# Performance work log

Hardware: AMD Instinct MI355X
Metric: run time of the kernel (lower is better)

## Reference

```python
import jax, jax.numpy as jnp
import numpy as np

B, S, I, H = 32, 1024, 128, 128
D = 2 * H  # bidirectional concat feature dim


def setup_inputs() -> dict:
    key = jax.random.key(0)
    ks = jax.random.split(key, 12)
    lim = 1.0 / np.sqrt(H)  # PyTorch LSTMCell uniform init bound
    u = lambda k, shape: jax.random.uniform(k, shape, jnp.float32, -lim, lim)
    x = jax.random.normal(ks[0], (B, S, I), jnp.float32)
    return {
        "x": x,
        "fw_Wih": u(ks[1], (4 * H, I)), "fw_Whh": u(ks[2], (4 * H, H)),
        "fw_bih": u(ks[3], (4 * H,)),   "fw_bhh": u(ks[4], (4 * H,)),
        "bw_Wih": u(ks[5], (4 * H, I)), "bw_Whh": u(ks[6], (4 * H, H)),
        "bw_bih": u(ks[7], (4 * H,)),   "bw_bhh": u(ks[8], (4 * H,)),
        "Wq": u(ks[9], (D, D)), "Wk": u(ks[10], (D, D)), "Wv": u(ks[11], (D, D)),
    }


def _lstm_dir(x, Wih, Whh, bih, bhh):
    # x: [B, S, I] -> hidden states [B, S, H]; PyTorch LSTMCell gate math.
    xg = jnp.einsum('bsi,gi->bsg', x, Wih) + bih + bhh  # precompute input projections

    def step(carry, xg_t):
        h, c = carry
        g = xg_t + h @ Whh.T
        i_, f_, g_, o_ = jnp.split(g, 4, axis=-1)
        c = jax.nn.sigmoid(f_) * c + jax.nn.sigmoid(i_) * jnp.tanh(g_)
        h = jax.nn.sigmoid(o_) * jnp.tanh(c)
        return (h, c), h

    h0 = jnp.zeros((x.shape[0], Whh.shape[1]), x.dtype)
    _, hs = jax.lax.scan(step, (h0, h0), jnp.swapaxes(xg, 0, 1))
    return jnp.swapaxes(hs, 0, 1)


def reference(x, fw_Wih, fw_Whh, fw_bih, fw_bhh,
              bw_Wih, bw_Whh, bw_bih, bw_bhh, Wq, Wk, Wv):
    f_h = _lstm_dir(x, fw_Wih, fw_Whh, fw_bih, fw_bhh)            # [B,S,H]
    b_h = _lstm_dir(x[:, ::-1, :], bw_Wih, bw_Whh, bw_bih, bw_bhh)[:, ::-1, :]
    h = jnp.concatenate([f_h, b_h], axis=2)                        # [B,S,2H]
    q = h @ Wq.T
    k = h @ Wk.T
    v = h @ Wv.T
    att = jnp.einsum('bsd,btd->bst', q, k) / jnp.sqrt(jnp.asarray(D, h.dtype))
    att = jax.nn.softmax(att, axis=2)
    return jnp.einsum('bst,btd->bsd', att, v)
```

## Files before the change

kernel.cpp:

```cpp
#include <hip/hip_runtime.h>

typedef unsigned short u16;
typedef unsigned int u32;
typedef __bf16 bf16x8 __attribute__((ext_vector_type(8)));
typedef bf16x8 __attribute__((may_alias)) bf16x8a;
typedef float f32x4 __attribute__((ext_vector_type(4)));
typedef _Float16 f16;
typedef _Float16 f16x2 __attribute__((ext_vector_type(2)));

#define BB 32
#define SS 1024
#define HH 128
#define DD 256

__device__ __forceinline__ float b2f(u16 u) {
    u32 v = ((u32)u) << 16;
    return __builtin_bit_cast(float, v);
}
__device__ __forceinline__ u16 f2b(float f) {
    u32 u = __builtin_bit_cast(u32, f);
    u32 r = (u + 0x7fffu + ((u >> 16) & 1u)) >> 16;
    return (u16)r;
}
__device__ __forceinline__ float sig_fast(float x) {
    return __builtin_amdgcn_rcpf(1.0f + __builtin_amdgcn_exp2f(-1.4426950408889634f * x));
}
__device__ __forceinline__ float tanh_fast(float x) {
    return 2.0f * sig_fast(2.0f * x) - 1.0f;
}
template <int CTRL>
__device__ __forceinline__ float dpp_xor(float x) {
    return __builtin_bit_cast(float,
        __builtin_amdgcn_update_dpp(0, __builtin_bit_cast(int, x),
                                    CTRL, 0xF, 0xF, true));
}
__device__ __forceinline__ void lds_barrier() {
    asm volatile("s_waitcnt lgkmcnt(0)\n\ts_barrier" ::: "memory");
}

__global__ __launch_bounds__(256) void conv_weights(
    const float* __restrict__ fwWih, const float* __restrict__ bwWih,
    const float* __restrict__ fwWhh, const float* __restrict__ bwWhh,
    const float* __restrict__ Wq, const float* __restrict__ Wk,
    const float* __restrict__ Wv,
    u16* __restrict__ wfih, u16* __restrict__ wbih, u16* __restrict__ whhf,
    u16* __restrict__ wq, u16* __restrict__ wk, u16* __restrict__ wv)
{
    const int which = blockIdx.y;
    const float* src; u16* dst; int mode;
    switch (which) {
        case 0: src = fwWih; dst = wfih;              mode = 0; break;
        case 1: src = bwWih; dst = wbih;              mode = 0; break;
        case 2: src = fwWhh; dst = whhf;              mode = 1; break;
        case 3: src = bwWhh; dst = whhf + 512 * 128;  mode = 1; break;
        case 4: src = Wq;    dst = wq;                mode = 2; break;
        case 5: src = Wk;    dst = wk;                mode = 2; break;
        default: src = Wv;   dst = wv;                mode = 2; break;
    }
    for (int i = blockIdx.x * 256 + threadIdx.x; i < 65536 / 4; i += 32 * 256) {
        float4 v = ((const float4*)src)[i];
        ushort4 o;
        if (mode == 1) {
            o.x = __builtin_bit_cast(u16, (f16)v.x);
            o.y = __builtin_bit_cast(u16, (f16)v.y);
            o.z = __builtin_bit_cast(u16, (f16)v.z);
            o.w = __builtin_bit_cast(u16, (f16)v.w);
        } else {
            o.x = f2b(v.x); o.y = f2b(v.y); o.z = f2b(v.z); o.w = f2b(v.w);
        }
        if (mode == 2) {
            ((ushort4*)dst)[i] = o;
        } else {
            int r = i >> 5, c4 = i & 31;
            int rp = ((r & 127) << 2) | (r >> 7);
            *(ushort4*)&dst[rp * 128 + c4 * 4] = o;
        }
    }
}

template <int MODE, int AFP32>
__device__ __forceinline__ void gemm_core(
    const void* __restrict__ Araw, const u16* __restrict__ Bt,
    const float* __restrict__ bias1, const float* __restrict__ bias2,
    u16* __restrict__ Cout, int K, int N)
{
    __shared__ u16 As[128 * 72];
    __shared__ u16 Bs[128 * 72];
    const int tid = threadIdx.x;
    const int lane = tid & 63, wave = tid >> 6;
    const int wm = wave >> 1, wn = wave & 1;
    const int lo = lane & 15, hi = lane >> 4;
    const int m0 = blockIdx.x * 128, n0 = blockIdx.y * 128;

    f32x4 acc[4][4] = {};

    for (int k0 = 0; k0 < K; k0 += 64) {
        __syncthreads();
#pragma unroll
        for (int i = 0; i < 4; i++) {
            int c = tid + 256 * i;
            int row = c >> 3, kc = (c & 7) * 8;
            if (AFP32) {
                const float* ap = (const float*)Araw + (size_t)(m0 + row) * K + k0 + kc;
                float4 v0 = *(const float4*)ap;
                float4 v1 = *(const float4*)(ap + 4);
                uint4 o;
                o.x = (u32)f2b(v0.x) | ((u32)f2b(v0.y) << 16);
                o.y = (u32)f2b(v0.z) | ((u32)f2b(v0.w) << 16);
                o.z = (u32)f2b(v1.x) | ((u32)f2b(v1.y) << 16);
                o.w = (u32)f2b(v1.z) | ((u32)f2b(v1.w) << 16);
                *(uint4*)&As[row * 72 + kc] = o;
            } else {
                *(uint4*)&As[row * 72 + kc] =
                    *(const uint4*)&((const u16*)Araw)[(size_t)(m0 + row) * K + k0 + kc];
            }
            *(uint4*)&Bs[row * 72 + kc] =
                *(const uint4*)&Bt[(size_t)(n0 + row) * K + k0 + kc];
        }
        __syncthreads();
#pragma unroll
        for (int ks = 0; ks < 2; ks++) {
            bf16x8 af[4], bfr[4];
#pragma unroll
            for (int i = 0; i < 4; i++)
                af[i] = *(const bf16x8a*)&As[(wm * 64 + i * 16 + lo) * 72 + ks * 32 + hi * 8];
#pragma unroll
            for (int j = 0; j < 4; j++)
                bfr[j] = *(const bf16x8a*)&Bs[(wn * 64 + j * 16 + lo) * 72 + ks * 32 + hi * 8];
#pragma unroll
            for (int i = 0; i < 4; i++)
#pragma unroll
                for (int j = 0; j < 4; j++)
                    acc[i][j] = __builtin_amdgcn_mfma_f32_16x16x32_bf16(
                        af[i], bfr[j], acc[i][j], 0, 0, 0);
        }
    }
#pragma unroll
    for (int j = 0; j < 4; j++) {
        int col = n0 + wn * 64 + j * 16 + lo;
        float bsum = 0.f;
        if (MODE == 1) {
            int co = ((col & 3) << 7) | (col >> 2);
            bsum = bias1[co] + bias2[co];
        }
#pragma unroll
        for (int i = 0; i < 4; i++) {
            int row0 = m0 + wm * 64 + i * 16 + hi * 4;
#pragma unroll
            for (int r = 0; r < 4; r++) {
                float v = acc[i][j][r] + bsum;
                if (MODE == 1) {
                    int row = row0 + r;
                    int sidx = row & 1023, bidx = row >> 10;
                    Cout[(size_t)sidx * (BB * 512) + bidx * 512 + col] = f2b(v);
                } else {
                    Cout[(size_t)(row0 + r) * N + col] = f2b(v);
                }
            }
        }
    }
}

__global__ __launch_bounds__(256) void gemm_xg(
    const float* __restrict__ A, const u16* __restrict__ Bt_f,
    const u16* __restrict__ Bt_b,
    const float* __restrict__ f_bih, const float* __restrict__ f_bhh,
    const float* __restrict__ b_bih, const float* __restrict__ b_bhh,
    u16* __restrict__ xg)
{
    const int dir = blockIdx.z;
    gemm_core<1, 1>(A, dir ? Bt_b : Bt_f,
                    dir ? b_bih : f_bih, dir ? b_bhh : f_bhh,
                    xg + (size_t)dir * SS * BB * 512, 128, 512);
}

__global__ __launch_bounds__(256) void gemm_qkv(
    const u16* __restrict__ A, const u16* __restrict__ Wq,
    const u16* __restrict__ Wk, const u16* __restrict__ Wv,
    u16* __restrict__ qb, u16* __restrict__ kb, u16* __restrict__ vb)
{
    const int z = blockIdx.z;
    const u16* Bt = (z == 0) ? Wq : (z == 1) ? Wk : Wv;
    u16* out = (z == 0) ? qb : (z == 1) ? kb : vb;
    gemm_core<0, 0>(A, Bt, nullptr, nullptr, out, 256, 256);
}

__global__ __launch_bounds__(256)
__attribute__((amdgpu_waves_per_eu(1, 1)))
void lstm_scan_sk(
    const u16* __restrict__ Whh_h,
    const u16* __restrict__ xg,
    u16* __restrict__ hout)
{
    const int wg = blockIdx.x;
    const int dir = wg >> 5, b = wg & 31;
    const int t_ = threadIdx.x;
    const int u = t_ >> 1;
    const int kh = t_ & 1;

    u32 w[4][32];
    {
        const volatile u32* vp = (const volatile u32*)(Whh_h + (size_t)dir * 512 * 128);
#pragma unroll
        for (int g = 0; g < 4; g++) {
            int base = ((4 * u + g) * 128 + kh * 64) >> 1;
#pragma unroll
            for (int k = 0; k < 32; k++) w[g][k] = vp[base + k];
        }
    }

    __shared__ __align__(16) u16 hbuf[2][128];
    if (t_ < 128) hbuf[0][t_] = 0;
    float c = 0.0f;

    const u16* xgp = xg + (size_t)dir * SS * (BB * 512) + (size_t)b * 512 + 4 * u;
    u16* hop = hout + (size_t)b * SS * DD + dir * HH + u;

    int s = dir ? (SS - 1) : 0;
    const int d1 = dir ? -1 : 1;
    uint2 nxA = *(const uint2*)&xgp[(size_t)s * (BB * 512)];
    uint2 nxB = *(const uint2*)&xgp[(size_t)(s + d1) * (BB * 512)];
    lds_barrier();

    auto body = [&](uint2& nx, int parity) {
        uint2 xv = nx;
        int sp = s + 2 * d1;
        if ((unsigned)sp < SS)
            nx = *(const uint2*)&xgp[(size_t)sp * (BB * 512)];

        const uint4* hb = (const uint4*)&hbuf[parity][kh * 64];
        float g0 = 0.f, g1 = 0.f, g2 = 0.f, g3 = 0.f;
#pragma unroll
        for (int cc = 0; cc < 8; cc++) {
            uint4 hh = hb[cc];
            u32 hv[4] = {hh.x, hh.y, hh.z, hh.w};
#pragma unroll
            for (int j = 0; j < 4; j++) {
                f16x2 hp = __builtin_bit_cast(f16x2, hv[j]);
                g0 = __builtin_amdgcn_fdot2(hp, __builtin_bit_cast(f16x2, w[0][4 * cc + j]), g0, false);
                g1 = __builtin_amdgcn_fdot2(hp, __builtin_bit_cast(f16x2, w[1][4 * cc + j]), g1, false);
                g2 = __builtin_amdgcn_fdot2(hp, __builtin_bit_cast(f16x2, w[2][4 * cc + j]), g2, false);
                g3 = __builtin_amdgcn_fdot2(hp, __builtin_bit_cast(f16x2, w[3][4 * cc + j]), g3, false);
            }
        }
        g0 += dpp_xor<0xB1>(g0);
        g1 += dpp_xor<0xB1>(g1);
        g2 += dpp_xor<0xB1>(g2);
        g3 += dpp_xor<0xB1>(g3);
        g0 += b2f((u16)(xv.x & 0xffff)); g1 += b2f((u16)(xv.x >> 16));
        g2 += b2f((u16)(xv.y & 0xffff)); g3 += b2f((u16)(xv.y >> 16));

        c = fmaf(sig_fast(g1), c, sig_fast(g0) * tanh_fast(g2));
        float h = sig_fast(g3) * tanh_fast(c);

        if (kh == 0)
            hbuf[parity ^ 1][u] = __builtin_bit_cast(u16, (f16)h);
        else
            hop[(size_t)s * DD] = f2b(h);
        lds_barrier();
        s += d1;
    };

    for (int t = 0; t < SS; t += 2) {
        body(nxA, 0);
        body(nxB, 1);
    }
}

__global__ __launch_bounds__(256) void transpose_v(
    const u16* __restrict__ v, u16* __restrict__ vT)
{
    __shared__ u16 tile[64 * 72];
    const int b = blockIdx.z, s0 = blockIdx.x * 64, d0 = blockIdx.y * 64;
    const int tid = threadIdx.x;
#pragma unroll
    for (int i = 0; i < 2; i++) {
        int c = tid + 256 * i;
        int sl = c >> 3, dc = (c & 7) * 8;
        *(uint4*)&tile[sl * 72 + dc] =
            *(const uint4*)&v[((size_t)b * SS + s0 + sl) * DD + d0 + dc];
    }
    __syncthreads();
#pragma unroll
    for (int i = 0; i < 2; i++) {
        int c = tid + 256 * i;
        int dl = c >> 3, sc = (c & 7) * 8;
        u32 x0 = (u32)tile[(sc + 0) * 72 + dl] | ((u32)tile[(sc + 1) * 72 + dl] << 16);
        u32 x1 = (u32)tile[(sc + 2) * 72 + dl] | ((u32)tile[(sc + 3) * 72 + dl] << 16);
        u32 x2 = (u32)tile[(sc + 4) * 72 + dl] | ((u32)tile[(sc + 5) * 72 + dl] << 16);
        u32 x3 = (u32)tile[(sc + 6) * 72 + dl] | ((u32)tile[(sc + 7) * 72 + dl] << 16);
        uint4 val; val.x = x0; val.y = x1; val.z = x2; val.w = x3;
        *(uint4*)&vT[((size_t)b * DD + d0 + dl) * SS + s0 + sc] = val;
    }
}

__global__ __launch_bounds__(256) void attn_kernel(
    const u16* __restrict__ q, const u16* __restrict__ k,
    const u16* __restrict__ vT, float* __restrict__ out)
{
    __shared__ u16 Ks[32 * 264];
    __shared__ u16 Vs[256 * 40];
    __shared__ u16 Ps[64 * 40];
    const int bid = blockIdx.x;
    const int b = (bid & 7) * 4 + (bid >> 7);
    const int q0 = ((bid >> 3) & 15) * 64;
    const int tid = threadIdx.x, wave = tid >> 6, lane = tid & 63;
    const int lo = lane & 15, hi = lane >> 4;
    const float c1 = 0.09016844005556021f;

    bf16x8 qf[8];
    {
        const u16* qp = q + ((size_t)b * SS + q0 + wave * 16 + lo) * DD;
#pragma unroll
        for (int ks = 0; ks < 8; ks++)
            qf[ks] = *(const bf16x8a*)&qp[ks * 32 + hi * 8];
    }
    float m_i[4] = {-1e30f, -1e30f, -1e30f, -1e30f};
    float l_i[4] = {0.f, 0.f, 0.f, 0.f};
    f32x4 o[16] = {};

    for (int t0 = 0; t0 < SS; t0 += 32) {
        __syncthreads();
#pragma unroll
        for (int i = 0; i < 4; i++) {
            int c = tid + 256 * i;
            {
                int row = c >> 5, dc = (c & 31) * 8;
                *(uint4*)&Ks[row * 264 + dc] =
                    *(const uint4*)&k[((size_t)b * SS + t0 + row) * DD + dc];
            }
            {
                int d = c >> 2, sc = (c & 3) * 8;
                *(uint4*)&Vs[d * 40 + sc] =
                    *(const uint4*)&vT[((size_t)b * DD + d) * SS + t0 + sc];
            }
        }
        __syncthreads();

        f32x4 sacc[2] = {};
#pragma unroll
        for (int ks = 0; ks < 8; ks++) {
#pragma unroll
            for (int j = 0; j < 2; j++) {
                bf16x8 bfr = *(const bf16x8a*)&Ks[(j * 16 + lo) * 264 + ks * 32 + hi * 8];
                sacc[j] = __builtin_amdgcn_mfma_f32_16x16x32_bf16(qf[ks], bfr, sacc[j], 0, 0, 0);
            }
        }

        float tt[2][4];
#pragma unroll
        for (int j = 0; j < 2; j++)
#pragma unroll
            for (int r = 0; r < 4; r++) tt[j][r] = sacc[j][r] * c1;
        float rm[4];
#pragma unroll
        for (int r = 0; r < 4; r++) rm[r] = fmaxf(tt[0][r], tt[1][r]);
#pragma unroll
        for (int mm = 1; mm <= 8; mm <<= 1)
#pragma unroll
            for (int r = 0; r < 4; r++) rm[r] = fmaxf(rm[r], __shfl_xor(rm[r], mm, 64));
        float al[4], rs[4];
#pragma unroll
        for (int r = 0; r < 4; r++) {
            float mn = fmaxf(m_i[r], rm[r]);
            al[r] = __builtin_amdgcn_exp2f(m_i[r] - mn);
            m_i[r] = mn;
            rs[r] = 0.f;
        }
#pragma unroll
        for (int j = 0; j < 2; j++)
#pragma unroll
            for (int r = 0; r < 4; r++) {
                float p = __builtin_amdgcn_exp2f(tt[j][r] - m_i[r]);
                rs[r] += p;
                Ps[(wave * 16 + hi * 4 + r) * 40 + j * 16 + lo] = f2b(p);
            }
#pragma unroll
        for (int mm = 1; mm <= 8; mm <<= 1)
#pragma unroll
            for (int r = 0; r < 4; r++) rs[r] += __shfl_xor(rs[r], mm, 64);
#pragma unroll
        for (int r = 0; r < 4; r++) l_i[r] = l_i[r] * al[r] + rs[r];
#pragma unroll
        for (int nt = 0; nt < 16; nt++) {
            o[nt][0] *= al[0]; o[nt][1] *= al[1];
            o[nt][2] *= al[2]; o[nt][3] *= al[3];
        }
        __syncthreads();
        bf16x8 pa = *(const bf16x8a*)&Ps[(wave * 16 + lo) * 40 + hi * 8];
#pragma unroll
        for (int nt = 0; nt < 16; nt++) {
            bf16x8 bv = *(const bf16x8a*)&Vs[(nt * 16 + lo) * 40 + hi * 8];
            o[nt] = __builtin_amdgcn_mfma_f32_16x16x32_bf16(pa, bv, o[nt], 0, 0, 0);
        }
    }
    float inv[4];
#pragma unroll
    for (int r = 0; r < 4; r++) inv[r] = __builtin_amdgcn_rcpf(l_i[r]);
#pragma unroll
    for (int nt = 0; nt < 16; nt++)
#pragma unroll
        for (int r = 0; r < 4; r++) {
            int row = q0 + wave * 16 + hi * 4 + r;
            int col = nt * 16 + lo;
            out[((size_t)b * SS + row) * DD + col] = o[nt][r] * inv[r];
        }
}

extern "C" void kernel_launch(void* const* d_in, const int* in_sizes, int n_in,
                              void* d_out, int out_size, void* d_ws, size_t ws_size,
                              hipStream_t stream)
{
    (void)in_sizes; (void)n_in; (void)out_size;
    const float* x      = (const float*)d_in[0];
    const float* fw_Wih = (const float*)d_in[1];
    const float* fw_Whh = (const float*)d_in[2];
    const float* fw_bih = (const float*)d_in[3];
    const float* fw_bhh = (const float*)d_in[4];
    const float* bw_Wih = (const float*)d_in[5];
    const float* bw_Whh = (const float*)d_in[6];
    const float* bw_bih = (const float*)d_in[7];
    const float* bw_bhh = (const float*)d_in[8];
    const float* Wq = (const float*)d_in[9];
    const float* Wk = (const float*)d_in[10];
    const float* Wv = (const float*)d_in[11];

    if (ws_size < 143523840ULL) return;

    char* ws = (char*)d_ws;
    u16* xg  = (u16*)ws;
    u16* h   = (u16*)(ws + 67108864);
    u16* qb  = (u16*)(ws + 83886080);
    u16* kb  = (u16*)(ws + 100663296);
    u16* vT  = (u16*)(ws + 117440512);
    u16* wfih16 = (u16*)(ws + 142606336);
    u16* wbih16 = (u16*)(ws + 142606336 + 131072);
    u16* wq16   = (u16*)(ws + 142606336 + 262144);
    u16* wk16   = (u16*)(ws + 142606336 + 393216);
    u16* wv16   = (u16*)(ws + 142606336 + 524288);
    u16* whhf16 = (u16*)(ws + 142606336 + 655360);
    u16* vb = (u16*)ws;

    conv_weights<<<dim3(32, 7), 256, 0, stream>>>(
        fw_Wih, bw_Wih, fw_Whh, bw_Whh, Wq, Wk, Wv,
        wfih16, wbih16, whhf16, wq16, wk16, wv16);

    gemm_xg<<<dim3(256, 4, 2), 256, 0, stream>>>(
        x, wfih16, wbih16, fw_bih, fw_bhh, bw_bih, bw_bhh, xg);
    lstm_scan_sk<<<64, 256, 0, stream>>>(whhf16, xg, h);
    gemm_qkv<<<dim3(256, 2, 3), 256, 0, stream>>>(h, wq16, wk16, wv16, qb, kb, vb);
    transpose_v<<<dim3(16, 4, 32), 256, 0, stream>>>(vb, vT);
    attn_kernel<<<512, 256, 0, stream>>>(qb, kb, vT, (float*)d_out);
}
```

Before: 764.8 us.

## Compute V transposed directly in QKV GEMM and drop transpose kernel

The V projection is now computed as Wv·hᵀ by swapping the GEMM operands and transposing the grid mapping, so it writes V in [D, B*S] layout directly. This removes the separate transpose_v kernel and its extra read and write of V, and the attention kernel's V load indexing is updated to match. It also raises wave priority around the MFMA loops in the attention kernel with s_setprio. The risk is poorer coalescing in the new V layout load and the priority hints interacting badly with scheduling.

Result: faster. 744.6 us (-2.6%).

```diff
diff --git a/kernel.cpp b/kernel.cpp
--- a/kernel.cpp
+++ b/kernel.cpp
@@ -78,7 +78,7 @@
     }
 }
 
-template <int MODE, int AFP32>
+template <int MODE, int AFP32, int TRANSGRID = 0>
 __device__ __forceinline__ void gemm_core(
     const void* __restrict__ Araw, const u16* __restrict__ Bt,
     const float* __restrict__ bias1, const float* __restrict__ bias2,
@@ -90,7 +90,8 @@
     const int lane = tid & 63, wave = tid >> 6;
     const int wm = wave >> 1, wn = wave & 1;
     const int lo = lane & 15, hi = lane >> 4;
-    const int m0 = blockIdx.x * 128, n0 = blockIdx.y * 128;
+    const int m0 = (TRANSGRID ? blockIdx.y : blockIdx.x) * 128;
+    const int n0 = (TRANSGRID ? blockIdx.x : blockIdx.y) * 128;
 
     f32x4 acc[4][4] = {};
 
@@ -177,12 +178,16 @@
 __global__ __launch_bounds__(256) void gemm_qkv(
     const u16* __restrict__ A, const u16* __restrict__ Wq,
     const u16* __restrict__ Wk, const u16* __restrict__ Wv,
-    u16* __restrict__ qb, u16* __restrict__ kb, u16* __restrict__ vb)
+    u16* __restrict__ qb, u16* __restrict__ kb, u16* __restrict__ vT)
 {
     const int z = blockIdx.z;
-    const u16* Bt = (z == 0) ? Wq : (z == 1) ? Wk : Wv;
-    u16* out = (z == 0) ? qb : (z == 1) ? kb : vb;
-    gemm_core<0, 0>(A, Bt, nullptr, nullptr, out, 256, 256);
+    if (z == 2) {
+        gemm_core<0, 0, 1>(Wv, A, nullptr, nullptr, vT, 256, BB * SS);
+    } else {
+        const u16* Bt = (z == 0) ? Wq : Wk;
+        u16* out = (z == 0) ? qb : kb;
+        gemm_core<0, 0>(A, Bt, nullptr, nullptr, out, 256, 256);
+    }
 }
 
 __global__ __launch_bounds__(256)
@@ -264,33 +269,6 @@
     for (int t = 0; t < SS; t += 2) {
         body(nxA, 0);
         body(nxB, 1);
-    }
-}
-
-__global__ __launch_bounds__(256) void transpose_v(
-    const u16* __restrict__ v, u16* __restrict__ vT)
-{
-    __shared__ u16 tile[64 * 72];
-    const int b = blockIdx.z, s0 = blockIdx.x * 64, d0 = blockIdx.y * 64;
-    const int tid = threadIdx.x;
-#pragma unroll
-    for (int i = 0; i < 2; i++) {
-        int c = tid + 256 * i;
-        int sl = c >> 3, dc = (c & 7) * 8;
-        *(uint4*)&tile[sl * 72 + dc] =
-            *(const uint4*)&v[((size_t)b * SS + s0 + sl) * DD + d0 + dc];
-    }
-    __syncthreads();
-#pragma unroll
-    for (int i = 0; i < 2; i++) {
-        int c = tid + 256 * i;
-        int dl = c >> 3, sc = (c & 7) * 8;
-        u32 x0 = (u32)tile[(sc + 0) * 72 + dl] | ((u32)tile[(sc + 1) * 72 + dl] << 16);
-        u32 x1 = (u32)tile[(sc + 2) * 72 + dl] | ((u32)tile[(sc + 3) * 72 + dl] << 16);
-        u32 x2 = (u32)tile[(sc + 4) * 72 + dl] | ((u32)tile[(sc + 5) * 72 + dl] << 16);
-        u32 x3 = (u32)tile[(sc + 6) * 72 + dl] | ((u32)tile[(sc + 7) * 72 + dl] << 16);
-        uint4 val; val.x = x0; val.y = x1; val.z = x2; val.w = x3;
-        *(uint4*)&vT[((size_t)b * DD + d0 + dl) * SS + s0 + sc] = val;
     }
 }
 
@@ -332,12 +310,13 @@
             {
                 int d = c >> 2, sc = (c & 3) * 8;
                 *(uint4*)&Vs[d * 40 + sc] =
-                    *(const uint4*)&vT[((size_t)b * DD + d) * SS + t0 + sc];
+                    *(const uint4*)&vT[(size_t)d * (BB * SS) + b * SS + t0 + sc];
             }
         }
         __syncthreads();
 
         f32x4 sacc[2] = {};
+        __builtin_amdgcn_s_setprio(1);
 #pragma unroll
         for (int ks = 0; ks < 8; ks++) {
 #pragma unroll
@@ -346,6 +325,7 @@
                 sacc[j] = __builtin_amdgcn_mfma_f32_16x16x32_bf16(qf[ks], bfr, sacc[j], 0, 0, 0);
             }
         }
+        __builtin_amdgcn_s_setprio(0);
 
         float tt[2][4];
 #pragma unroll
@@ -388,11 +368,13 @@
         }
         __syncthreads();
         bf16x8 pa = *(const bf16x8a*)&Ps[(wave * 16 + lo) * 40 + hi * 8];
+        __builtin_amdgcn_s_setprio(1);
 #pragma unroll
         for (int nt = 0; nt < 16; nt++) {
             bf16x8 bv = *(const bf16x8a*)&Vs[(nt * 16 + lo) * 40 + hi * 8];
             o[nt] = __builtin_amdgcn_mfma_f32_16x16x32_bf16(pa, bv, o[nt], 0, 0, 0);
         }
+        __builtin_amdgcn_s_setprio(0);
     }
     float inv[4];
 #pragma unroll
@@ -439,7 +421,6 @@
     u16* wk16   = (u16*)(ws + 142606336 + 393216);
     u16* wv16   = (u16*)(ws + 142606336 + 524288);
     u16* whhf16 = (u16*)(ws + 142606336 + 655360);
-    u16* vb = (u16*)ws;
 
     conv_weights<<<dim3(32, 7), 256, 0, stream>>>(
         fw_Wih, bw_Wih, fw_Whh, bw_Whh, Wq, Wk, Wv,
@@ -448,7 +429,6 @@
     gemm_xg<<<dim3(256, 4, 2), 256, 0, stream>>>(
         x, wfih16, wbih16, fw_bih, fw_bhh, bw_bih, bw_bhh, xg);
     lstm_scan_sk<<<64, 256, 0, stream>>>(whhf16, xg, h);
-    gemm_qkv<<<dim3(256, 2, 3), 256, 0, stream>>>(h, wq16, wk16, wv16, qb, kb, vb);
-    transpose_v<<<dim3(16, 4, 32), 256, 0, stream>>>(vb, vT);
+    gemm_qkv<<<dim3(256, 2, 3), 256, 0, stream>>>(h, wq16, wk16, wv16, qb, kb, vT);
     attn_kernel<<<512, 256, 0, stream>>>(qb, kb, vT, (float*)d_out);
 }
```
